# Performance work log

Measured on AMD Instinct MI355X. Metric: run time of the kernel, lower is better.

## Reference

```python
import jax, jax.numpy as jnp
import numpy as np

T, B, I, H, C, O = 4096, 8, 256, 512, 1024, 512
SCHEDULE = 1.0
UPPER_T = 0.3
NIND = int((1.0 - SCHEDULE) * (C - 2) * UPPER_T) + 1  # = 1 (argmax WTA)


def setup_inputs() -> dict:
    key = jax.random.key(0)
    ks = jax.random.split(key, 8)
    def lin(k, fan_out, fan_in):
        s = 1.0 / np.sqrt(fan_in)
        kw, kb = jax.random.split(k)
        return (jax.random.uniform(kw, (fan_out, fan_in), jnp.float32, -s, s),
                jax.random.uniform(kb, (fan_out,), jnp.float32, -s, s))
    i2m_w, i2m_b = lin(ks[0], H, I)
    m2h_w, m2h_b = lin(ks[1], C, H)
    h2o_w, h2o_b = lin(ks[2], O, C)
    return {
        "x": jax.random.normal(ks[3], (T, B, I), jnp.float32),
        "hidden1": jnp.zeros((1,), jnp.float32),  # unused dummy (overwritten in torch forward)
        "i2m_w": i2m_w, "i2m_b": i2m_b,
        "m2h_w": m2h_w, "m2h_b": m2h_b,
        "h2o_w": h2o_w, "h2o_b": h2o_b,
    }


def reference(x, hidden1, i2m_w, i2m_b, m2h_w, m2h_b, h2o_w, h2o_b):
    # linear -> relu
    h = jax.nn.relu(jnp.einsum('tbi,hi->tbh', x, i2m_w) + i2m_b)
    # linear -> relu -> concept pre-activations [T,B,C]
    c = jax.nn.relu(jnp.einsum('tbh,ch->tbc', h, m2h_w) + m2h_b)
    # winner-take-all: top-Nind scatter mask (replaces CPU argsort round-trip)
    _, idx = jax.lax.top_k(c, NIND)  # [T,B,NIND]
    t_ix = jnp.arange(c.shape[0])[:, None, None]
    b_ix = jnp.arange(c.shape[1])[None, :, None]
    mask = jnp.zeros_like(c).at[t_ix, b_ix, idx].set(1.0)
    m = c * mask
    # L2 normalize over concept axis
    m = m / jnp.linalg.norm(m, axis=-1, keepdims=True)
    out = jnp.einsum('tbc,oc->tbo', m, h2o_w) + h2o_b
    return jax.nn.log_softmax(out, axis=-1)
```

## Files before the change

### kernel.cpp

```cpp
#include <hip/hip_runtime.h>
#include <stdint.h>

#define M_ROWS 32768
#define I_DIM 256
#define H_DIM 512
#define C_DIM 1024
#define O_DIM 512

typedef __attribute__((ext_vector_type(8))) short bf16x8;
typedef __attribute__((ext_vector_type(4))) float f32x4;

__device__ __forceinline__ ushort bf16_rne(float f) {
    unsigned u = __float_as_uint(f);
    unsigned r = u + 0x7FFFu + ((u >> 16) & 1u);
    return (ushort)(r >> 16);
}
__device__ __forceinline__ float bf16_f32(ushort h) {
    return __uint_as_float(((unsigned)h) << 16);
}
__device__ __forceinline__ void split2(float f, ushort& hi, ushort& mid) {
    hi = bf16_rne(f);
    mid = bf16_rne(f - bf16_f32(hi));
}

__device__ __forceinline__ void async_ld16(const void* g, void* l) {
    __builtin_amdgcn_global_load_lds(
        (const __attribute__((address_space(1))) void*)g,
        (__attribute__((address_space(3))) void*)l, 16, 0, 0);
}

__device__ __forceinline__ unsigned long long packvi(float v, int col) {
    unsigned u = __float_as_uint(v);
    u = (u & 0x80000000u) ? ~u : (u | 0x80000000u);
    return ((unsigned long long)u << 32) | (unsigned)(~col);
}

__global__ __launch_bounds__(256)
void prep(const float* __restrict__ W1, ushort* __restrict__ w1h, ushort* __restrict__ w1m,
          const float* __restrict__ W2, ushort* __restrict__ w2h, ushort* __restrict__ w2m,
          const float* __restrict__ Wo, const float* __restrict__ bo,
          float* __restrict__ LS, unsigned long long* __restrict__ part) {
    __shared__ float sred[4];
    const int b = blockIdx.x;
    const int t = threadIdx.x;
    if (b < 640) {
        const float* W = (b < 128) ? W1 : W2;
        ushort* hh = (b < 128) ? w1h : w2h;
        ushort* mm = (b < 128) ? w1m : w2m;
        int i = ((b < 128 ? b : b - 128) * 256 + t) * 4;
        float4 v = *(const float4*)(W + i);
        ushort4 hv, mv;
        split2(v.x, hv.x, mv.x);
        split2(v.y, hv.y, mv.y);
        split2(v.z, hv.z, mv.z);
        split2(v.w, hv.w, mv.w);
        *(ushort4*)(hh + i) = hv;
        *(ushort4*)(mm + i) = mv;
    } else if (b < 1664) {
        const int j = b - 640;
        float l0 = Wo[(size_t)t * C_DIM + j] + bo[t];
        float l1 = Wo[(size_t)(t + 256) * C_DIM + j] + bo[t + 256];

        float mx = fmaxf(l0, l1);
        #pragma unroll
        for (int off = 1; off < 64; off <<= 1)
            mx = fmaxf(mx, __shfl_xor(mx, off, 64));
        if ((t & 63) == 0) sred[t >> 6] = mx;
        __syncthreads();
        mx = fmaxf(fmaxf(sred[0], sred[1]), fmaxf(sred[2], sred[3]));
        __syncthreads();

        float s = expf(l0 - mx) + expf(l1 - mx);
        #pragma unroll
        for (int off = 1; off < 64; off <<= 1)
            s += __shfl_xor(s, off, 64);
        if ((t & 63) == 0) sred[t >> 6] = s;
        __syncthreads();
        s = sred[0] + sred[1] + sred[2] + sred[3];

        float lse = mx + logf(s);
        LS[(size_t)j * O_DIM + t] = l0 - lse;
        LS[(size_t)j * O_DIM + t + 256] = l1 - lse;
    } else {
        part[(b - 1664) * 256 + t] = 0ull;
    }
}

__global__ __launch_bounds__(256, 4)
void gemm1_mfma(const float* __restrict__ X, const ushort* __restrict__ W1h,
                const ushort* __restrict__ W1m, const float* __restrict__ b1,
                ushort* __restrict__ Hh, ushort* __restrict__ Hm) {
    __shared__ __align__(16) ushort As[2][128 * 32];
    __shared__ __align__(16) ushort Bs[2][128 * 32];
    const int tid = threadIdx.x;
    const int lane = tid & 63, wave = tid >> 6;
    const int wm = wave >> 1, wn = wave & 1;
    const int lcol = lane & 15, quad = lane >> 4;
    const int mBase = blockIdx.x * 128;
    const int nBase = blockIdx.y * 128;
    const int s_row = tid >> 1, s_half = tid & 1;
    const int bplane = wave >> 1;
    const ushort* wp = bplane ? W1m : W1h;
    const int brow0 = (wave & 1) * 64;
    const int lrow = lane >> 2, lk = (lane & 3) * 8;

    f32x4 acc[4][4];
    #pragma unroll
    for (int i = 0; i < 4; ++i)
        #pragma unroll
        for (int j = 0; j < 4; ++j)
            acc[i][j] = (f32x4){0.f, 0.f, 0.f, 0.f};

    int aoff[4], boff[4];
    #pragma unroll
    for (int t = 0; t < 4; ++t) {
        aoff[t] = (wm * 64 + t * 16 + lcol) * 32 + quad * 8;
        boff[t] = (wn * 64 + t * 16 + lcol) * 32 + quad * 8;
    }

    for (int ks = 0; ks < I_DIM / 32; ++ks) {
        const int k0 = ks * 32;
        const float* ap = X + (size_t)(mBase + s_row) * I_DIM + k0 + s_half * 16;
        float4 f0 = ((const float4*)ap)[0];
        float4 f1 = ((const float4*)ap)[1];
        float4 f2 = ((const float4*)ap)[2];
        float4 f3 = ((const float4*)ap)[3];

        __syncthreads();

        #pragma unroll
        for (int i = 0; i < 4; ++i) {
            int r = brow0 + i * 16;
            const ushort* g = wp + (size_t)(nBase + r + lrow) * I_DIM + k0 + lk;
            async_ld16(g, &Bs[bplane][r * 32]);
        }

        float f[16];
        *(float4*)&f[0] = f0; *(float4*)&f[4] = f1;
        *(float4*)&f[8] = f2; *(float4*)&f[12] = f3;
        bf16x8 h0, h1, m0, m1;
        #pragma unroll
        for (int j = 0; j < 8; ++j) {
            ushort hu, mu;
            split2(f[j], hu, mu);
            h0[j] = (short)hu; m0[j] = (short)mu;
            split2(f[j + 8], hu, mu);
            h1[j] = (short)hu; m1[j] = (short)mu;
        }
        int dst = s_row * 32 + s_half * 16;
        int sw = (s_row >> 1) & 1;
        *(bf16x8*)&As[0][dst + sw * 8]     = sw ? h1 : h0;
        *(bf16x8*)&As[0][dst + 8 - sw * 8] = sw ? h0 : h1;
        *(bf16x8*)&As[1][dst + sw * 8]     = sw ? m1 : m0;
        *(bf16x8*)&As[1][dst + 8 - sw * 8] = sw ? m0 : m1;

        __syncthreads();

        bf16x8 af[4][2];
        #pragma unroll
        for (int mt = 0; mt < 4; ++mt) {
            af[mt][0] = *(const bf16x8*)&As[0][aoff[mt]];
            af[mt][1] = *(const bf16x8*)&As[1][aoff[mt]];
        }
        #pragma unroll
        for (int nt = 0; nt < 4; ++nt) {
            bf16x8 bh = *(const bf16x8*)&Bs[0][boff[nt]];
            bf16x8 bm = *(const bf16x8*)&Bs[1][boff[nt]];
            #pragma unroll
            for (int mt = 0; mt < 4; ++mt) {
                f32x4 a = acc[mt][nt];
                a = __builtin_amdgcn_mfma_f32_16x16x32_bf16(af[mt][1], bh, a, 0, 0, 0);
                a = __builtin_amdgcn_mfma_f32_16x16x32_bf16(af[mt][0], bm, a, 0, 0, 0);
                a = __builtin_amdgcn_mfma_f32_16x16x32_bf16(af[mt][0], bh, a, 0, 0, 0);
                acc[mt][nt] = a;
            }
        }
    }

    #pragma unroll
    for (int nt = 0; nt < 4; ++nt) {
        int col = nBase + wn * 64 + nt * 16 + lcol;
        float bias = b1[col];
        #pragma unroll
        for (int mt = 0; mt < 4; ++mt) {
            #pragma unroll
            for (int r = 0; r < 4; ++r) {
                int row = mBase + wm * 64 + mt * 16 + quad * 4 + r;
                float v = fmaxf(acc[mt][nt][r] + bias, 0.f);
                ushort hu, mu;
                split2(v, hu, mu);
                Hh[(size_t)row * H_DIM + col] = hu;
                Hm[(size_t)row * H_DIM + col] = mu;
            }
        }
    }
}

__global__ __launch_bounds__(256, 4)
void gemm2_mfma(const ushort* __restrict__ Hh, const ushort* __restrict__ Hm,
                const ushort* __restrict__ W2h, const ushort* __restrict__ W2m,
                const float* __restrict__ b2,
                unsigned long long* __restrict__ part) {
    __shared__ __align__(16) ushort As[2][128 * 32];
    __shared__ __align__(16) ushort Bs[2][128 * 32];
    const int tid = threadIdx.x;
    const int lane = tid & 63, wave = tid >> 6;
    const int wm = wave >> 1, wn = wave & 1;
    const int lcol = lane & 15, quad = lane >> 4;
    const int mBase = blockIdx.x * 128;
    const int nBase = blockIdx.y * 128;
    const int lrow = lane >> 2, lk = (lane & 3) * 8;

    const ushort* gsrc;
    ushort* lbase;
    switch (wave) {
        case 0: gsrc = Hh  + (size_t)mBase * H_DIM; lbase = As[0]; break;
        case 1: gsrc = Hm  + (size_t)mBase * H_DIM; lbase = As[1]; break;
        case 2: gsrc = W2h + (size_t)nBase * H_DIM; lbase = Bs[0]; break;
        default: gsrc = W2m + (size_t)nBase * H_DIM; lbase = Bs[1]; break;
    }

    f32x4 acc[4][4];
    #pragma unroll
    for (int i = 0; i < 4; ++i)
        #pragma unroll
        for (int j = 0; j < 4; ++j)
            acc[i][j] = (f32x4){0.f, 0.f, 0.f, 0.f};

    int aoff[4], boff[4];
    #pragma unroll
    for (int t = 0; t < 4; ++t) {
        aoff[t] = (wm * 64 + t * 16 + lcol) * 32 + quad * 8;
        boff[t] = (wn * 64 + t * 16 + lcol) * 32 + quad * 8;
    }

    for (int ks = 0; ks < H_DIM / 32; ++ks) {
        const int k0 = ks * 32;
        __syncthreads();
        #pragma unroll
        for (int j = 0; j < 8; ++j) {
            const ushort* g = gsrc + (size_t)(j * 16 + lrow) * H_DIM + k0 + lk;
            async_ld16(g, lbase + j * 512);
        }
        __syncthreads();

        bf16x8 af[4][2];
        #pragma unroll
        for (int mt = 0; mt < 4; ++mt) {
            af[mt][0] = *(const bf16x8*)&As[0][aoff[mt]];
            af[mt][1] = *(const bf16x8*)&As[1][aoff[mt]];
        }
        #pragma unroll
        for (int nt = 0; nt < 4; ++nt) {
            bf16x8 bh = *(const bf16x8*)&Bs[0][boff[nt]];
            bf16x8 bm = *(const bf16x8*)&Bs[1][boff[nt]];
            #pragma unroll
            for (int mt = 0; mt < 4; ++mt) {
                f32x4 a = acc[mt][nt];
                a = __builtin_amdgcn_mfma_f32_16x16x32_bf16(af[mt][1], bh, a, 0, 0, 0);
                a = __builtin_amdgcn_mfma_f32_16x16x32_bf16(af[mt][0], bm, a, 0, 0, 0);
                a = __builtin_amdgcn_mfma_f32_16x16x32_bf16(af[mt][0], bh, a, 0, 0, 0);
                acc[mt][nt] = a;
            }
        }
    }

    #pragma unroll
    for (int mt = 0; mt < 4; ++mt) {
        #pragma unroll
        for (int r = 0; r < 4; ++r) {
            unsigned long long best = 0ull;
            #pragma unroll
            for (int nt = 0; nt < 4; ++nt) {
                int col = nBase + wn * 64 + nt * 16 + lcol;
                float v = acc[mt][nt][r] + b2[col];
                unsigned long long p = packvi(v, col);
                if (p > best) best = p;
            }
            #pragma unroll
            for (int off = 1; off < 16; off <<= 1) {
                unsigned long long o = __shfl_xor((long long)best, off, 64);
                if (o > best) best = o;
            }
            if (lcol == 0) {
                int row = mBase + wm * 64 + mt * 16 + quad * 4 + r;
                atomicMax(&part[row], best);
            }
        }
    }
}

__global__ __launch_bounds__(256)
void gather_out(const unsigned long long* __restrict__ part,
                const float* __restrict__ LS, float* __restrict__ out) {
    const int tid = threadIdx.x;
    const int row = blockIdx.x * 2 + (tid >> 7);
    const int q = tid & 127;
    unsigned long long best = part[row];
    unsigned u = (unsigned)(best >> 32);
    float v = (u & 0x80000000u) ? __uint_as_float(u ^ 0x80000000u)
                                : __uint_as_float(~u);
    int col = (int)(~(unsigned)best) & (C_DIM - 1);
    int j = (v > 0.f) ? col : 0;
    float4 val = ((const float4*)LS)[(size_t)j * 128 + q];
    ((float4*)out)[(size_t)row * 128 + q] = val;
}

extern "C" void kernel_launch(void* const* d_in, const int* in_sizes, int n_in,
                              void* d_out, int out_size, void* d_ws, size_t ws_size,
                              hipStream_t stream) {
    const float* x     = (const float*)d_in[0];
    const float* i2m_w = (const float*)d_in[2];
    const float* i2m_b = (const float*)d_in[3];
    const float* m2h_w = (const float*)d_in[4];
    const float* m2h_b = (const float*)d_in[5];
    const float* h2o_w = (const float*)d_in[6];
    const float* h2o_b = (const float*)d_in[7];
    float* out = (float*)d_out;

    char* ws = (char*)d_ws;
    ushort* w1h = (ushort*)(ws);
    ushort* w1m = (ushort*)(ws + 262144);
    ushort* w2h = (ushort*)(ws + 524288);
    ushort* w2m = (ushort*)(ws + 1572864);
    float*  LS  = (float*)(ws + 2621440);
    unsigned long long* part = (unsigned long long*)(ws + 4718592);

    ushort* Hh = (ushort*)d_out;
    ushort* Hm = Hh + (size_t)M_ROWS * H_DIM;

    prep<<<1792, 256, 0, stream>>>(i2m_w, w1h, w1m, m2h_w, w2h, w2m,
                                   h2o_w, h2o_b, LS, part);
    gemm1_mfma<<<dim3(M_ROWS / 128, H_DIM / 128), 256, 0, stream>>>(
        x, w1h, w1m, i2m_b, Hh, Hm);
    gemm2_mfma<<<dim3(M_ROWS / 128, C_DIM / 128), 256, 0, stream>>>(
        Hh, Hm, w2h, w2m, m2h_b, part);
    gather_out<<<M_ROWS / 2, 256, 0, stream>>>(part, LS, out);
}
```

Before: 260.4 us.

## Swizzle LDS tiles via pre-swizzled global layout and stage gemm1 epilogue stores

Introduces a 4-slot XOR-like swizzle of 8-element chunks within each 32-wide k group. W1/W2 and the H activations are written to global memory already swizzled, so the direct global-to-LDS async loads land in a bank-conflict-reduced layout and the fragment reads use the matching slot offsets. The gemm1 epilogue now stages each plane through LDS and writes coalesced 16-byte rows instead of scattered 2-byte stores. This adds extra barriers and LDS traffic in the epilogue and relies on every producer and consumer agreeing on the swizzle.

Measured after the change: 253.5 us. -2.7%, faster.

```diff
diff --git a/kernel.cpp b/kernel.cpp
--- a/kernel.cpp
+++ b/kernel.cpp
@@ -33,6 +33,10 @@
     unsigned u = __float_as_uint(v);
     u = (u & 0x80000000u) ? ~u : (u | 0x80000000u);
     return ((unsigned long long)u << 32) | (unsigned)(~col);
+}
+
+__device__ __forceinline__ int slot_of(int kc, int row) {
+    return (kc + ((row >> 1) & 3)) & 3;
 }
 
 __global__ __launch_bounds__(256)
@@ -43,21 +47,29 @@
     __shared__ float sred[4];
     const int b = blockIdx.x;
     const int t = threadIdx.x;
-    if (b < 640) {
-        const float* W = (b < 128) ? W1 : W2;
-        ushort* hh = (b < 128) ? w1h : w2h;
-        ushort* mm = (b < 128) ? w1m : w2m;
-        int i = ((b < 128 ? b : b - 128) * 256 + t) * 4;
-        float4 v = *(const float4*)(W + i);
-        ushort4 hv, mv;
-        split2(v.x, hv.x, mv.x);
-        split2(v.y, hv.y, mv.y);
-        split2(v.z, hv.z, mv.z);
-        split2(v.w, hv.w, mv.w);
-        *(ushort4*)(hh + i) = hv;
-        *(ushort4*)(mm + i) = mv;
-    } else if (b < 1664) {
-        const int j = b - 640;
+    if (b < 320) {
+        const int isW1 = (b < 64);
+        const float* W = isW1 ? W1 : W2;
+        ushort* hh = isW1 ? w1h : w2h;
+        ushort* mm = isW1 ? w1m : w2m;
+        const int K = isW1 ? I_DIM : H_DIM;
+        const int cpr = K >> 3;
+        int gid = (isW1 ? b : b - 64) * 256 + t;
+        int row = gid / cpr;
+        int rem = gid - row * cpr;
+        int g = rem >> 2, kc = rem & 3;
+        float4 v0 = *(const float4*)(W + (size_t)gid * 8);
+        float4 v1 = *(const float4*)(W + (size_t)gid * 8 + 4);
+        __align__(16) ushort h[8], m[8];
+        float f[8];
+        *(float4*)&f[0] = v0; *(float4*)&f[4] = v1;
+        #pragma unroll
+        for (int j = 0; j < 8; ++j) split2(f[j], h[j], m[j]);
+        size_t dst = (size_t)row * K + g * 32 + slot_of(kc, row) * 8;
+        *(uint4*)(hh + dst) = *(uint4*)h;
+        *(uint4*)(mm + dst) = *(uint4*)m;
+    } else if (b < 1344) {
+        const int j = b - 320;
         float l0 = Wo[(size_t)t * C_DIM + j] + bo[t];
         float l1 = Wo[(size_t)(t + 256) * C_DIM + j] + bo[t + 256];
 
@@ -82,7 +94,7 @@
         LS[(size_t)j * O_DIM + t] = l0 - lse;
         LS[(size_t)j * O_DIM + t + 256] = l1 - lse;
     } else {
-        part[(b - 1664) * 256 + t] = 0ull;
+        part[(b - 1344) * 256 + t] = 0ull;
     }
 }
 
@@ -90,8 +102,12 @@
 void gemm1_mfma(const float* __restrict__ X, const ushort* __restrict__ W1h,
                 const ushort* __restrict__ W1m, const float* __restrict__ b1,
                 ushort* __restrict__ Hh, ushort* __restrict__ Hm) {
-    __shared__ __align__(16) ushort As[2][128 * 32];
-    __shared__ __align__(16) ushort Bs[2][128 * 32];
+    __shared__ __align__(16) ushort LB[16384];
+    ushort* As0 = LB;
+    ushort* As1 = LB + 4096;
+    ushort* Bs0 = LB + 8192;
+    ushort* Bs1 = LB + 12288;
+
     const int tid = threadIdx.x;
     const int lane = tid & 63, wave = tid >> 6;
     const int wm = wave >> 1, wn = wave & 1;
@@ -114,9 +130,13 @@
     int aoff[4], boff[4];
     #pragma unroll
     for (int t = 0; t < 4; ++t) {
-        aoff[t] = (wm * 64 + t * 16 + lcol) * 32 + quad * 8;
-        boff[t] = (wn * 64 + t * 16 + lcol) * 32 + quad * 8;
-    }
+        int ra = wm * 64 + t * 16 + lcol;
+        int rb = wn * 64 + t * 16 + lcol;
+        aoff[t] = ra * 32 + slot_of(quad, ra) * 8;
+        boff[t] = rb * 32 + slot_of(quad, rb) * 8;
+    }
+    const int sl0 = slot_of(s_half * 2,     s_row);
+    const int sl1 = slot_of(s_half * 2 + 1, s_row);
 
     for (int ks = 0; ks < I_DIM / 32; ++ks) {
         const int k0 = ks * 32;
@@ -132,7 +152,7 @@
         for (int i = 0; i < 4; ++i) {
             int r = brow0 + i * 16;
             const ushort* g = wp + (size_t)(nBase + r + lrow) * I_DIM + k0 + lk;
-            async_ld16(g, &Bs[bplane][r * 32]);
+            async_ld16(g, (bplane ? Bs1 : Bs0) + r * 32);
         }
 
         float f[16];
@@ -147,25 +167,23 @@
             split2(f[j + 8], hu, mu);
             h1[j] = (short)hu; m1[j] = (short)mu;
         }
-        int dst = s_row * 32 + s_half * 16;
-        int sw = (s_row >> 1) & 1;
-        *(bf16x8*)&As[0][dst + sw * 8]     = sw ? h1 : h0;
-        *(bf16x8*)&As[0][dst + 8 - sw * 8] = sw ? h0 : h1;
-        *(bf16x8*)&As[1][dst + sw * 8]     = sw ? m1 : m0;
-        *(bf16x8*)&As[1][dst + 8 - sw * 8] = sw ? m0 : m1;
+        *(bf16x8*)&As0[s_row * 32 + sl0 * 8] = h0;
+        *(bf16x8*)&As0[s_row * 32 + sl1 * 8] = h1;
+        *(bf16x8*)&As1[s_row * 32 + sl0 * 8] = m0;
+        *(bf16x8*)&As1[s_row * 32 + sl1 * 8] = m1;
 
         __syncthreads();
 
         bf16x8 af[4][2];
         #pragma unroll
         for (int mt = 0; mt < 4; ++mt) {
-            af[mt][0] = *(const bf16x8*)&As[0][aoff[mt]];
-            af[mt][1] = *(const bf16x8*)&As[1][aoff[mt]];
+            af[mt][0] = *(const bf16x8*)&As0[aoff[mt]];
+            af[mt][1] = *(const bf16x8*)&As1[aoff[mt]];
         }
         #pragma unroll
         for (int nt = 0; nt < 4; ++nt) {
-            bf16x8 bh = *(const bf16x8*)&Bs[0][boff[nt]];
-            bf16x8 bm = *(const bf16x8*)&Bs[1][boff[nt]];
+            bf16x8 bh = *(const bf16x8*)&Bs0[boff[nt]];
+            bf16x8 bm = *(const bf16x8*)&Bs1[boff[nt]];
             #pragma unroll
             for (int mt = 0; mt < 4; ++mt) {
                 f32x4 a = acc[mt][nt];
@@ -178,20 +196,34 @@
     }
 
     #pragma unroll
-    for (int nt = 0; nt < 4; ++nt) {
-        int col = nBase + wn * 64 + nt * 16 + lcol;
-        float bias = b1[col];
-        #pragma unroll
-        for (int mt = 0; mt < 4; ++mt) {
-            #pragma unroll
-            for (int r = 0; r < 4; ++r) {
-                int row = mBase + wm * 64 + mt * 16 + quad * 4 + r;
-                float v = fmaxf(acc[mt][nt][r] + bias, 0.f);
-                ushort hu, mu;
-                split2(v, hu, mu);
-                Hh[(size_t)row * H_DIM + col] = hu;
-                Hm[(size_t)row * H_DIM + col] = mu;
-            }
+    for (int plane = 0; plane < 2; ++plane) {
+        __syncthreads();
+        #pragma unroll
+        for (int nt = 0; nt < 4; ++nt) {
+            int colRel = wn * 64 + nt * 16 + lcol;
+            int g = colRel >> 5, kc = (colRel >> 3) & 3, pos = colRel & 7;
+            float bias = b1[nBase + colRel];
+            #pragma unroll
+            for (int mt = 0; mt < 4; ++mt) {
+                #pragma unroll
+                for (int r = 0; r < 4; ++r) {
+                    int rowRel = wm * 64 + mt * 16 + quad * 4 + r;
+                    float v = fmaxf(acc[mt][nt][r] + bias, 0.f);
+                    ushort hu, mu;
+                    split2(v, hu, mu);
+                    LB[rowRel * 128 + g * 32 + slot_of(kc, rowRel) * 8 + pos]
+                        = plane ? mu : hu;
+                }
+            }
+        }
+        __syncthreads();
+        ushort* dstp = plane ? Hm : Hh;
+        #pragma unroll
+        for (int l = 0; l < 8; ++l) {
+            int c = l * 256 + tid;
+            int row = c >> 4, idx = c & 15;
+            *(uint4*)(dstp + (size_t)(mBase + row) * H_DIM + nBase + idx * 8)
+                = *(const uint4*)&LB[row * 128 + idx * 8];
         }
     }
 }
@@ -230,8 +262,10 @@
     int aoff[4], boff[4];
     #pragma unroll
     for (int t = 0; t < 4; ++t) {
-        aoff[t] = (wm * 64 + t * 16 + lcol) * 32 + quad * 8;
-        boff[t] = (wn * 64 + t * 16 + lcol) * 32 + quad * 8;
+        int ra = wm * 64 + t * 16 + lcol;
+        int rb = wn * 64 + t * 16 + lcol;
+        aoff[t] = ra * 32 + slot_of(quad, ra) * 8;
+        boff[t] = rb * 32 + slot_of(quad, rb) * 8;
     }
 
     for (int ks = 0; ks < H_DIM / 32; ++ks) {
@@ -329,7 +363,7 @@
     ushort* Hh = (ushort*)d_out;
     ushort* Hm = Hh + (size_t)M_ROWS * H_DIM;
 
-    prep<<<1792, 256, 0, stream>>>(i2m_w, w1h, w1m, m2h_w, w2h, w2m,
+    prep<<<1472, 256, 0, stream>>>(i2m_w, w1h, w1m, m2h_w, w2h, w2m,
                                    h2o_w, h2o_b, LS, part);
     gemm1_mfma<<<dim3(M_ROWS / 128, H_DIM / 128), 256, 0, stream>>>(
         x, w1h, w1m, i2m_b, Hh, Hm);
```
